# Kernel tuning notes

Hardware: AMD Instinct MI355X
Metric: run time of the kernel (lower is better)

Reference implementation:

```python
import jax, jax.numpy as jnp
import numpy as np

N = 100000
E = 1600000
D_IN = 128
D_OUT = 128

def setup_inputs() -> dict:
    key = jax.random.key(0)
    k1, k2, k3, k4, k5, k6 = jax.random.split(key, 6)
    h = jax.random.normal(k1, (N, D_IN), dtype=jnp.float32)
    # norm ~ deg^{-1/2}; use positive uniform values as stand-in
    norm = jax.random.uniform(k2, (N, 1), dtype=jnp.float32, minval=0.05, maxval=1.0)
    src = jax.random.randint(k3, (E,), 0, N, dtype=jnp.int32)
    dst = jax.random.randint(k4, (E,), 0, N, dtype=jnp.int32)
    weight = jax.random.normal(k5, (D_IN, D_OUT), dtype=jnp.float32) * (2.0 / (D_IN + D_OUT)) ** 0.5
    bias = jnp.zeros((D_OUT,), dtype=jnp.float32)
    return {"h": h, "norm": norm, "src": src, "dst": dst, "weight": weight, "bias": bias}

def reference(h, norm, src, dst, weight, bias):
    n_nodes = h.shape[0]
    hw = h @ weight                      # [N, D_out] dense GEMM
    hw = hw * norm                       # pre-aggregation degree scale
    msgs = hw[src]                       # gather: [E, D_out]
    agg = jax.ops.segment_sum(msgs, dst, num_segments=n_nodes)  # scatter-sum
    out = agg * norm + bias              # post-scale + bias
    return out
```

## Files before the change

### kernel.cpp

```cpp
#include <hip/hip_runtime.h>
#include <hip/hip_bf16.h>
#include <hip/hip_cooperative_groups.h>

namespace cg = cooperative_groups;

#define D 128
#define D4 32
#define CHUNK 6400
#define MAXB 2048
#define NSEG 8
#define SL 4096

typedef __attribute__((ext_vector_type(8))) short bf16x8;
typedef __attribute__((ext_vector_type(8))) unsigned short ushort8;
typedef __attribute__((ext_vector_type(4))) float f32x4;

static __device__ __forceinline__ unsigned short f2bf(float f) {
    unsigned u = __float_as_uint(f);
    u += 0x7FFFu + ((u >> 16) & 1u);
    return (unsigned short)(u >> 16);
}
static __device__ __forceinline__ float bf2f(unsigned short u) {
    return __uint_as_float(((unsigned)u) << 16);
}

__global__ __launch_bounds__(256) void wcvt_kernel(
    const float* __restrict__ W, unsigned short* __restrict__ Wt)
{
    const int idx = blockIdx.x * 256 + threadIdx.x;
    const float4 w = ((const float4*)W)[idx];
    const int k = idx >> 5;
    const int c = (idx & 31) * 4;
    Wt[(c + 0) * 128 + k] = f2bf(w.x);
    Wt[(c + 1) * 128 + k] = f2bf(w.y);
    Wt[(c + 2) * 128 + k] = f2bf(w.z);
    Wt[(c + 3) * 128 + k] = f2bf(w.w);
}

__global__ __launch_bounds__(512) void gemm_mfma_kernel(
    const float* __restrict__ h, const unsigned short* __restrict__ Wt,
    const float* __restrict__ norm, unsigned short* __restrict__ hwb,
    int n_nodes)
{
    __shared__ unsigned short Bs[128 * 136];

    const int t = threadIdx.x;
    const int row0 = blockIdx.x * 128;

    #pragma unroll
    for (int i = 0; i < 4; ++i) {
        const int idx = t + 512 * i;
        const int c = idx >> 4;
        const int k8 = idx & 15;
        *(ushort8*)&Bs[c * 136 + k8 * 8] = ((const ushort8*)Wt)[idx];
    }
    __syncthreads();

    const int wv = t >> 6;
    const int lane = t & 63;
    const int m = lane & 15;
    const int quad = lane >> 4;

    long gra = row0 + wv * 16 + m;
    if (gra >= n_nodes) gra = n_nodes - 1;
    const float* hrow = h + gra * D;

    f32x4 acc[8];
    #pragma unroll
    for (int nt = 0; nt < 8; ++nt) { f32x4 z = {0.f, 0.f, 0.f, 0.f}; acc[nt] = z; }

    #pragma unroll
    for (int kt = 0; kt < 4; ++kt) {
        const float4 a0 = *(const float4*)(hrow + kt * 32 + quad * 8);
        const float4 a1 = *(const float4*)(hrow + kt * 32 + quad * 8 + 4);
        bf16x8 af;
        unsigned short* ap = (unsigned short*)&af;
        ap[0] = f2bf(a0.x); ap[1] = f2bf(a0.y); ap[2] = f2bf(a0.z); ap[3] = f2bf(a0.w);
        ap[4] = f2bf(a1.x); ap[5] = f2bf(a1.y); ap[6] = f2bf(a1.z); ap[7] = f2bf(a1.w);
        #pragma unroll
        for (int nt = 0; nt < 8; ++nt) {
            const bf16x8 bfr = *(const bf16x8*)&Bs[(nt * 16 + m) * 136 + kt * 32 + quad * 8];
            acc[nt] = __builtin_amdgcn_mfma_f32_16x16x32_bf16(af, bfr, acc[nt], 0, 0, 0);
        }
    }

    float nv[4];
    #pragma unroll
    for (int i = 0; i < 4; ++i) {
        const int gr = row0 + wv * 16 + quad * 4 + i;
        nv[i] = (gr < n_nodes) ? norm[gr] : 0.f;
    }

    __syncthreads();
    #pragma unroll
    for (int nt = 0; nt < 8; ++nt) {
        #pragma unroll
        for (int i = 0; i < 4; ++i) {
            const int r = wv * 16 + quad * 4 + i;
            Bs[r * 136 + nt * 16 + m] = f2bf(acc[nt][i] * nv[i]);
        }
    }
    __syncthreads();

    #pragma unroll
    for (int i2 = 0; i2 < 4; ++i2) {
        const int idx = t + 512 * i2;
        const int r = idx >> 4;
        const int c8 = idx & 15;
        const int gr = row0 + r;
        if (gr < n_nodes)
            *(ushort8*)&hwb[(size_t)gr * D + c8 * 8] =
                *(const ushort8*)&Bs[r * 136 + c8 * 8];
    }
}

__global__ __launch_bounds__(1024) void coop_edge_kernel(
    const int* __restrict__ src, const int* __restrict__ dst,
    int* __restrict__ H, int* __restrict__ PS, int* __restrict__ SB,
    int* __restrict__ boff, int* __restrict__ CO,
    unsigned int* __restrict__ ebuf, int* __restrict__ srcs_g,
    const unsigned short* __restrict__ hwb,
    const float* __restrict__ norm, const float* __restrict__ bias,
    float* __restrict__ out,
    int n_edges, int n_nodes, int EB, int NBUCK)
{
    __shared__ int smem[SL + 192];

    cg::grid_group grid = cg::this_grid();
    const int t = threadIdx.x;
    const int g = blockIdx.x;
    const int gid = g * 1024 + t;
    const int glen = (EB + NSEG - 1) / NSEG;
    const int e0 = g * CHUNK;
    const int e1 = min(e0 + CHUNK, n_edges);

    {
        int* lbh = smem;
        for (int i = t; i < MAXB; i += 1024) lbh[i] = 0;
        if (g == 0 && t < 32) {
            ushort4 z; z.x = z.y = z.z = z.w = 0;
            ((ushort4*)(hwb + (size_t)n_nodes * D))[t] = z;
        }
        __syncthreads();
        for (int e = e0 + t; e < e1; e += 1024)
            atomicAdd(&lbh[dst[e] >> 6], 1);
        __syncthreads();
        for (int i = t; i < MAXB; i += 1024) H[(size_t)g * MAXB + i] = lbh[i];
    }
    grid.sync();

    if (gid < NSEG * MAXB) {
        const int seg = gid >> 11;
        const int c = gid & (MAXB - 1);
        const int g0 = seg * glen, g1 = min(g0 + glen, EB);
        int s = 0;
        for (int gg = g0; gg < g1; ++gg) s += H[(size_t)gg * MAXB + c];
        PS[seg * MAXB + c] = s;
    }
    grid.sync();

    if (g == 0) {
        int* tmp = smem;
        const int cA = 2 * t, cB = 2 * t + 1;
        int va = 0, vb = 0;
        #pragma unroll
        for (int sg = 0; sg < NSEG; ++sg) { va += PS[sg * MAXB + cA]; vb += PS[sg * MAXB + cB]; }
        tmp[t] = va + vb;
        __syncthreads();
        for (int ofs = 1; ofs < 1024; ofs <<= 1) {
            const int x = (t >= ofs) ? tmp[t - ofs] : 0;
            __syncthreads();
            tmp[t] += x;
            __syncthreads();
        }
        const int run = tmp[t] - (va + vb);
        boff[cA] = run;
        boff[cB] = run + va;
        if (t == 1023) boff[MAXB] = tmp[1023];
        int sb = run;
        #pragma unroll
        for (int sg = 0; sg < NSEG; ++sg) { SB[sg * MAXB + cA] = sb; sb += PS[sg * MAXB + cA]; }
        sb = run + va;
        #pragma unroll
        for (int sg = 0; sg < NSEG; ++sg) { SB[sg * MAXB + cB] = sb; sb += PS[sg * MAXB + cB]; }
    }
    grid.sync();

    if (gid < NSEG * MAXB) {
        const int seg = gid >> 11;
        const int c = gid & (MAXB - 1);
        const int g0 = seg * glen, g1 = min(g0 + glen, EB);
        int run = SB[seg * MAXB + c];
        for (int gg = g0; gg < g1; ++gg) {
            CO[(size_t)gg * MAXB + c] = run;
            run += H[(size_t)gg * MAXB + c];
        }
    }
    grid.sync();

    {
        int* lbh = smem;
        int* lofs = smem + MAXB;
        for (int i = t; i < MAXB; i += 1024) {
            lbh[i] = 0;
            lofs[i] = CO[(size_t)g * MAXB + i];
        }
        __syncthreads();
        for (int e = e0 + t; e < e1; e += 1024) {
            const int d = dst[e];
            const int bk = d >> 6;
            const int r = atomicAdd(&lbh[bk], 1);
            ebuf[lofs[bk] + r] = (unsigned)src[e] | ((unsigned)(d & 63) << 17);
        }
    }
    grid.sync();

    {
        int* slds = smem;
        int* lcnt = smem + SL;
        int* lcur = smem + SL + 64;
        int* loff = smem + SL + 128;
        const ushort4* hw4 = (const ushort4*)hwb;
        const int grp = t >> 5;
        const int l = t & 31;
        const float4 bs = ((const float4*)bias)[l];

        for (int bkt = g; bkt < NBUCK; bkt += gridDim.x) {
            __syncthreads();
            if (t < 64) lcnt[t] = 0;
            __syncthreads();
            const int w0 = boff[bkt], w1 = boff[bkt + 1];
            const int wlen = w1 - w0;
            const bool uselds = (wlen + 480) <= SL;
            const int gbase = w0 + 448 * bkt;
            const int gn0 = bkt * 64;

            for (int e = w0 + t; e < w1; e += 1024)
                atomicAdd(&lcnt[(ebuf[e] >> 17) & 63], 1);
            __syncthreads();
            if (t < 64) {
                const int c = lcnt[t];
                const int p = (c + 7) & ~7;
                int x = p;
                #pragma unroll
                for (int ofs = 1; ofs < 64; ofs <<= 1) {
                    const int y = __shfl_up(x, ofs, 64);
                    if (t >= ofs) x += y;
                }
                const int base = x - p;
                lcur[t] = base;
                loff[t] = base;
            }
            __syncthreads();
            for (int e = w0 + t; e < w1; e += 1024) {
                const unsigned rec = ebuf[e];
                const int loc = (rec >> 17) & 63;
                const int pos = atomicAdd(&lcur[loc], 1);
                const int sv = (int)(rec & 0x1FFFFu);
                if (uselds) slds[pos] = sv; else srcs_g[gbase + pos] = sv;
            }
            for (int w = t; w < 512; w += 1024) {
                const int ln = w >> 3, k = w & 7;
                const int gn = gn0 + ln;
                if (gn < n_nodes) {
                    const int c = lcnt[ln];
                    const int pad = (8 - (c & 7)) & 7;
                    if (k < pad) {
                        const int pos = loff[ln] + c + k;
                        if (uselds) slds[pos] = n_nodes; else srcs_g[gbase + pos] = n_nodes;
                    }
                }
            }
            __syncthreads();

            #pragma unroll
            for (int nn = 0; nn < 2; ++nn) {
                const int loc = grp * 2 + nn;
                const int gn = gn0 + loc;
                if (gn >= n_nodes) continue;
                const int start = loff[loc];
                const int deg = lcnt[loc];
                const int nb8 = (deg + 7) >> 3;
                float4 acc; acc.x = acc.y = acc.z = acc.w = 0.f;
                int myidx = 0;
                for (int bb = 0; bb < nb8; ++bb) {
                    const int q = bb & 3;
                    if (q == 0) {
                        const int ri = start + bb * 8 + l;
                        myidx = uselds ? slds[ri] : srcs_g[gbase + ri];
                    }
                    ushort4 v[8];
                    #pragma unroll
                    for (int jj = 0; jj < 8; ++jj) {
                        const int s = __shfl(myidx, q * 8 + jj, 32);
                        v[jj] = hw4[(long)s * D4 + l];
                    }
                    #pragma unroll
                    for (int jj = 0; jj < 8; ++jj) {
                        acc.x += bf2f(v[jj].x);
                        acc.y += bf2f(v[jj].y);
                        acc.z += bf2f(v[jj].z);
                        acc.w += bf2f(v[jj].w);
                    }
                }
                const float nv = norm[gn];
                float4 o;
                o.x = acc.x * nv + bs.x;
                o.y = acc.y * nv + bs.y;
                o.z = acc.z * nv + bs.z;
                o.w = acc.w * nv + bs.w;
                ((float4*)out)[(long)gn * D4 + l] = o;
            }
        }
    }
}

__global__ __launch_bounds__(1024) void hist_kernel(
    const int* __restrict__ dst, int* __restrict__ H,
    unsigned short* __restrict__ hwb, int n_edges, int n_nodes)
{
    __shared__ int lbh[MAXB];
    const int t = threadIdx.x;
    const int g = blockIdx.x;
    for (int i = t; i < MAXB; i += 1024) lbh[i] = 0;
    if (g == 0 && t < 32) {
        ushort4 z; z.x = z.y = z.z = z.w = 0;
        ((ushort4*)(hwb + (size_t)n_nodes * D))[t] = z;
    }
    __syncthreads();
    const int e0 = g * CHUNK;
    const int e1 = min(e0 + CHUNK, n_edges);
    for (int e = e0 + t; e < e1; e += 1024) {
        atomicAdd(&lbh[dst[e] >> 6], 1);
    }
    __syncthreads();
    for (int i = t; i < MAXB; i += 1024) {
        H[(size_t)g * MAXB + i] = lbh[i];
    }
}

__global__ __launch_bounds__(256) void chunkscan_local_kernel(
    const int* __restrict__ H, int* __restrict__ CO, int* __restrict__ PS,
    int eb)
{
    const int b = blockIdx.x * 256 + threadIdx.x;
    const int seg = blockIdx.y;
    const int glen = (eb + NSEG - 1) / NSEG;
    const int g0 = seg * glen;
    const int g1 = min(g0 + glen, eb);
    int run = 0;
    for (int g = g0; g < g1; ++g) {
        CO[(size_t)g * MAXB + b] = run;
        run += H[(size_t)g * MAXB + b];
    }
    PS[seg * MAXB + b] = run;
}

__global__ __launch_bounds__(256) void bucket_scan_kernel(
    const int* __restrict__ PS, int* __restrict__ boff, int* __restrict__ SB)
{
    __shared__ int tmp[256];
    const int t = threadIdx.x;
    int v[8];
    int s = 0;
    #pragma unroll
    for (int k = 0; k < 8; ++k) {
        const int i = t * 8 + k;
        int c = 0;
        #pragma unroll
        for (int sg = 0; sg < NSEG; ++sg) c += PS[sg * MAXB + i];
        v[k] = c; s += c;
    }
    tmp[t] = s;
    __syncthreads();
    for (int ofs = 1; ofs < 256; ofs <<= 1) {
        int x = (t >= ofs) ? tmp[t - ofs] : 0;
        __syncthreads();
        tmp[t] += x;
        __syncthreads();
    }
    int run = tmp[t] - s;
    #pragma unroll
    for (int k = 0; k < 8; ++k) {
        const int i = t * 8 + k;
        boff[i] = run;
        int sb = run;
        #pragma unroll
        for (int sg = 0; sg < NSEG; ++sg) {
            SB[sg * MAXB + i] = sb;
            sb += PS[sg * MAXB + i];
        }
        run += v[k];
    }
    if (t == 255) boff[MAXB] = run;
}

__global__ __launch_bounds__(1024) void bscatter_kernel(
    const int* __restrict__ src, const int* __restrict__ dst,
    const int* __restrict__ CO, const int* __restrict__ SB,
    unsigned int* __restrict__ ebuf, int n_edges, int eb)
{
    __shared__ int lbh[MAXB];
    __shared__ int lofs[MAXB];
    const int t = threadIdx.x;
    const int g = blockIdx.x;
    const int glen = (eb + NSEG - 1) / NSEG;
    const int seg = g / glen;
    for (int i = t; i < MAXB; i += 1024) {
        lbh[i] = 0;
        lofs[i] = SB[seg * MAXB + i] + CO[(size_t)g * MAXB + i];
    }
    __syncthreads();
    const int e0 = g * CHUNK;
    const int e1 = min(e0 + CHUNK, n_edges);
    for (int e = e0 + t; e < e1; e += 1024) {
        const int d = dst[e];
        const int bk = d >> 6;
        const int r = atomicAdd(&lbh[bk], 1);
        ebuf[lofs[bk] + r] = (unsigned)src[e] | ((unsigned)(d & 63) << 17);
    }
}

__global__ __launch_bounds__(256) void fillagg_kernel(
    const unsigned int* __restrict__ ebuf, const int* __restrict__ boff,
    int* __restrict__ srcs_g, const unsigned short* __restrict__ hwb,
    const float* __restrict__ norm, const float* __restrict__ bias,
    float* __restrict__ out, int n_nodes)
{
    __shared__ int slds[SL];
    __shared__ int lcnt[64];
    __shared__ int lcur[64];
    __shared__ int loff[64];
    const int t = threadIdx.x;
    const int b = blockIdx.x;
    const int gn0 = b * 64;

    if (t < 64) lcnt[t] = 0;
    __syncthreads();
    const int w0 = boff[b], w1 = boff[b + 1];
    const int wlen = w1 - w0;
    const bool uselds = (wlen + 480) <= SL;
    const int gbase = w0 + 448 * b;

    for (int e = w0 + t; e < w1; e += 256) {
        atomicAdd(&lcnt[(ebuf[e] >> 17) & 63], 1);
    }
    __syncthreads();
    if (t < 64) {
        const int c = lcnt[t];
        const int p = (c + 7) & ~7;
        int x = p;
        #pragma unroll
        for (int ofs = 1; ofs < 64; ofs <<= 1) {
            const int y = __shfl_up(x, ofs, 64);
            if (t >= ofs) x += y;
        }
        const int base = x - p;
        lcur[t] = base;
        loff[t] = base;
    }
    __syncthreads();
    for (int e = w0 + t; e < w1; e += 256) {
        const unsigned rec = ebuf[e];
        const int loc = (rec >> 17) & 63;
        const int pos = atomicAdd(&lcur[loc], 1);
        const int sv = (int)(rec & 0x1FFFFu);
        if (uselds) slds[pos] = sv; else srcs_g[gbase + pos] = sv;
    }
    for (int w = t; w < 512; w += 256) {
        const int ln = w >> 3, k = w & 7;
        const int gn = gn0 + ln;
        if (gn < n_nodes) {
            const int c = lcnt[ln];
            const int pad = (8 - (c & 7)) & 7;
            if (k < pad) {
                const int pos = loff[ln] + c + k;
                if (uselds) slds[pos] = n_nodes; else srcs_g[gbase + pos] = n_nodes;
            }
        }
    }
    __syncthreads();

    const ushort4* hw4 = (const ushort4*)hwb;
    const int grp = t >> 5;
    const int l = t & 31;
    const float4 bs = ((const float4*)bias)[l];
    for (int nn = 0; nn < 8; ++nn) {
        const int loc = grp * 8 + nn;
        const int gn = gn0 + loc;
        if (gn >= n_nodes) continue;
        const int start = loff[loc];
        const int deg = lcnt[loc];
        const int nb8 = (deg + 7) >> 3;
        float4 acc; acc.x = acc.y = acc.z = acc.w = 0.f;
        int myidx = 0;
        for (int bb = 0; bb < nb8; ++bb) {
            const int q = bb & 3;
            if (q == 0) {
                const int ri = start + bb * 8 + l;
                myidx = uselds ? slds[ri] : srcs_g[gbase + ri];
            }
            ushort4 v[8];
            #pragma unroll
            for (int jj = 0; jj < 8; ++jj) {
                const int s = __shfl(myidx, q * 8 + jj, 32);
                v[jj] = hw4[(long)s * D4 + l];
            }
            #pragma unroll
            for (int jj = 0; jj < 8; ++jj) {
                acc.x += bf2f(v[jj].x);
                acc.y += bf2f(v[jj].y);
                acc.z += bf2f(v[jj].z);
                acc.w += bf2f(v[jj].w);
            }
        }
        const float nv = norm[gn];
        float4 o;
        o.x = acc.x * nv + bs.x;
        o.y = acc.y * nv + bs.y;
        o.z = acc.z * nv + bs.z;
        o.w = acc.w * nv + bs.w;
        ((float4*)out)[(long)gn * D4 + l] = o;
    }
}

__global__ __launch_bounds__(256) void scatter_kernel(
    const unsigned short* __restrict__ hwb, const int* __restrict__ src,
    const int* __restrict__ dst, float* __restrict__ out, int n_edges)
{
    const int idx = blockIdx.x * 256 + threadIdx.x;
    if (idx >= n_edges * D4) return;
    const int e = idx >> 5;
    const int g = idx & 31;
    const int s = src[e];
    const int d = dst[e];
    const ushort4 v = ((const ushort4*)hwb)[(long)s * D4 + g];
    float* o = out + (long)d * D + g * 4;
    atomicAdd(o + 0, bf2f(v.x));
    atomicAdd(o + 1, bf2f(v.y));
    atomicAdd(o + 2, bf2f(v.z));
    atomicAdd(o + 3, bf2f(v.w));
}

__global__ __launch_bounds__(256) void finalize_kernel(
    float* __restrict__ out, const float* __restrict__ norm,
    const float* __restrict__ bias, int n_nodes)
{
    const int idx = blockIdx.x * 256 + threadIdx.x;
    if (idx >= n_nodes * D4) return;
    const int n = idx >> 5;
    const int g = idx & 31;
    float4 v = ((float4*)out)[idx];
    const float nv = norm[n];
    const float4 b = ((const float4*)bias)[g];
    v.x = v.x * nv + b.x;
    v.y = v.y * nv + b.y;
    v.z = v.z * nv + b.z;
    v.w = v.w * nv + b.w;
    ((float4*)out)[idx] = v;
}

extern "C" void kernel_launch(void* const* d_in, const int* in_sizes, int n_in,
                              void* d_out, int out_size, void* d_ws, size_t ws_size,
                              hipStream_t stream) {
    const float* h    = (const float*)d_in[0];
    const float* norm = (const float*)d_in[1];
    const int*   src  = (const int*)d_in[2];
    const int*   dst  = (const int*)d_in[3];
    const float* W    = (const float*)d_in[4];
    const float* bias = (const float*)d_in[5];
    float* out = (float*)d_out;

    const int n_nodes = in_sizes[1];
    const int n_edges = in_sizes[2];

    const int NBUCK = (n_nodes + 63) >> 6;
    const int EB    = (n_edges + CHUNK - 1) / CHUNK;
    const int srcs_len = n_edges + 448 * NBUCK + 64;

    size_t p = 0;
    auto take = [&](size_t bytes) {
        size_t cur = p;
        p += (bytes + 255) & ~(size_t)255;
        return cur;
    };
    const size_t hwb_off  = take(((size_t)n_nodes + 1) * D * sizeof(unsigned short));
    const size_t wt_off   = take((size_t)D * D * sizeof(unsigned short));
    const size_t srcs_off = take((size_t)srcs_len * sizeof(int));
    const size_t ebuf_off = take((size_t)n_edges * sizeof(unsigned int));
    const size_t boff_off = take((MAXB + 1) * sizeof(int));
    const size_t H_off    = take((size_t)EB * MAXB * sizeof(int));
    const size_t PS_off   = take((size_t)NSEG * MAXB * sizeof(int));
    const size_t SB_off   = take((size_t)NSEG * MAXB * sizeof(int));
    const size_t CO_off   = take((size_t)EB * MAXB * sizeof(int));
    const size_t needed = p;

    char* ws = (char*)d_ws;
    unsigned short* hwb = (unsigned short*)(ws + hwb_off);
    unsigned short* Wt  = (unsigned short*)(ws + wt_off);

    wcvt_kernel<<<16, 256, 0, stream>>>(W, Wt);
    gemm_mfma_kernel<<<(n_nodes + 127) / 128, 512, 0, stream>>>(h, Wt, norm, hwb, n_nodes);

    static int s_max_coop_blocks = -1;
    if (s_max_coop_blocks < 0) {
        int nb = 0;
        if (hipOccupancyMaxActiveBlocksPerMultiprocessor(&nb, coop_edge_kernel, 1024, 0)
            != hipSuccess) nb = 0;
        int dev = 0;
        hipGetDevice(&dev);
        int ncu = 0;
        if (hipDeviceGetAttribute(&ncu, hipDeviceAttributeMultiprocessorCount, dev)
            != hipSuccess) ncu = 0;
        s_max_coop_blocks = nb * ncu;
    }

    const bool ws_ok = (ws_size >= needed) && (NBUCK <= MAXB) && (n_nodes <= 131072);
    const bool coop_ok = ws_ok && EB >= 16 && EB <= 512 && EB <= s_max_coop_blocks;

    if (coop_ok) {
        int* srcs  = (int*)(ws + srcs_off);
        unsigned int* ebuf = (unsigned int*)(ws + ebuf_off);
        int* boff  = (int*)(ws + boff_off);
        int* H     = (int*)(ws + H_off);
        int* PS    = (int*)(ws + PS_off);
        int* SBp   = (int*)(ws + SB_off);
        int* CO    = (int*)(ws + CO_off);

        int ne = n_edges, nn = n_nodes, eb = EB, nbk = NBUCK;
        void* args[] = {
            (void*)&src, (void*)&dst, (void*)&H, (void*)&PS, (void*)&SBp,
            (void*)&boff, (void*)&CO, (void*)&ebuf, (void*)&srcs, (void*)&hwb,
            (void*)&norm, (void*)&bias, (void*)&out,
            (void*)&ne, (void*)&nn, (void*)&eb, (void*)&nbk
        };
        hipLaunchCooperativeKernel((void*)coop_edge_kernel, dim3(EB), dim3(1024),
                                   args, 0, stream);
    } else if (ws_ok && EB <= 1024) {
        int* srcs  = (int*)(ws + srcs_off);
        unsigned int* ebuf = (unsigned int*)(ws + ebuf_off);
        int* boff  = (int*)(ws + boff_off);
        int* H     = (int*)(ws + H_off);
        int* PS    = (int*)(ws + PS_off);
        int* SBp   = (int*)(ws + SB_off);
        int* CO    = (int*)(ws + CO_off);

        hist_kernel<<<EB, 1024, 0, stream>>>(dst, H, hwb, n_edges, n_nodes);
        chunkscan_local_kernel<<<dim3(MAXB / 256, NSEG), 256, 0, stream>>>(H, CO, PS, EB);
        bucket_scan_kernel<<<1, 256, 0, stream>>>(PS, boff, SBp);
        bscatter_kernel<<<EB, 1024, 0, stream>>>(src, dst, CO, SBp, ebuf, n_edges, EB);
        fillagg_kernel<<<NBUCK, 256, 0, stream>>>(ebuf, boff, srcs, hwb, norm, bias,
                                                  out, n_nodes);
    } else {
        hipMemsetAsync(d_out, 0, (size_t)out_size * sizeof(float), stream);
        const int work = n_edges * D4;
        scatter_kernel<<<(work + 255) / 256, 256, 0, stream>>>(hwb, src, dst, out, n_edges);
        const int work2 = n_nodes * D4;
        finalize_kernel<<<(work2 + 255) / 256, 256, 0, stream>>>(out, norm, bias, n_nodes);
    }
}
```

Measured before the change: 227.4 us.

## Keep edge records in registers across grid syncs and drop CO pass

Edges are now loaded once into registers during the histogram phase, and the LDS atomic rank is kept so the scatter phase needs neither a second read of src/dst nor a second atomic pass. The separate chunk-offset pass, its CO buffer and one grid.sync are removed: each block rebuilds its own offsets by summing H over earlier blocks in its segment. In the bucket phase, records read from ebuf are also held in registers between the count and place steps. Float-to-bf16 conversion now uses a packed two-value intrinsic. In exchange, register pressure rises and per-block offset work grows with segment length. All of this assumes CHUNK fits in KSLOT*1024 edges and each bucket in 4096 records.

```diff
diff --git a/kernel.cpp b/kernel.cpp
--- a/kernel.cpp
+++ b/kernel.cpp
@@ -7,6 +7,7 @@
 #define D 128
 #define D4 32
 #define CHUNK 6400
+#define KSLOT 7
 #define MAXB 2048
 #define NSEG 8
 #define SL 4096
@@ -15,13 +16,13 @@
 typedef __attribute__((ext_vector_type(8))) unsigned short ushort8;
 typedef __attribute__((ext_vector_type(4))) float f32x4;
 
-static __device__ __forceinline__ unsigned short f2bf(float f) {
-    unsigned u = __float_as_uint(f);
-    u += 0x7FFFu + ((u >> 16) & 1u);
-    return (unsigned short)(u >> 16);
-}
 static __device__ __forceinline__ float bf2f(unsigned short u) {
     return __uint_as_float(((unsigned)u) << 16);
+}
+static __device__ __forceinline__ unsigned pk2(float x, float y) {
+    float2 f; f.x = x; f.y = y;
+    __hip_bfloat162 b = __float22bfloat162_rn(f);
+    return *(unsigned*)&b;
 }
 
 __global__ __launch_bounds__(256) void wcvt_kernel(
@@ -31,10 +32,12 @@
     const float4 w = ((const float4*)W)[idx];
     const int k = idx >> 5;
     const int c = (idx & 31) * 4;
-    Wt[(c + 0) * 128 + k] = f2bf(w.x);
-    Wt[(c + 1) * 128 + k] = f2bf(w.y);
-    Wt[(c + 2) * 128 + k] = f2bf(w.z);
-    Wt[(c + 3) * 128 + k] = f2bf(w.w);
+    const unsigned q01 = pk2(w.x, w.y);
+    const unsigned q23 = pk2(w.z, w.w);
+    Wt[(c + 0) * 128 + k] = (unsigned short)(q01 & 0xFFFFu);
+    Wt[(c + 1) * 128 + k] = (unsigned short)(q01 >> 16);
+    Wt[(c + 2) * 128 + k] = (unsigned short)(q23 & 0xFFFFu);
+    Wt[(c + 3) * 128 + k] = (unsigned short)(q23 >> 16);
 }
 
 __global__ __launch_bounds__(512) void gemm_mfma_kernel(
@@ -74,9 +77,11 @@
         const float4 a0 = *(const float4*)(hrow + kt * 32 + quad * 8);
         const float4 a1 = *(const float4*)(hrow + kt * 32 + quad * 8 + 4);
         bf16x8 af;
-        unsigned short* ap = (unsigned short*)&af;
-        ap[0] = f2bf(a0.x); ap[1] = f2bf(a0.y); ap[2] = f2bf(a0.z); ap[3] = f2bf(a0.w);
-        ap[4] = f2bf(a1.x); ap[5] = f2bf(a1.y); ap[6] = f2bf(a1.z); ap[7] = f2bf(a1.w);
+        unsigned* aw = (unsigned*)&af;
+        aw[0] = pk2(a0.x, a0.y);
+        aw[1] = pk2(a0.z, a0.w);
+        aw[2] = pk2(a1.x, a1.y);
+        aw[3] = pk2(a1.z, a1.w);
         #pragma unroll
         for (int nt = 0; nt < 8; ++nt) {
             const bf16x8 bfr = *(const bf16x8*)&Bs[(nt * 16 + m) * 136 + kt * 32 + quad * 8];
@@ -94,11 +99,13 @@
     __syncthreads();
     #pragma unroll
     for (int nt = 0; nt < 8; ++nt) {
-        #pragma unroll
-        for (int i = 0; i < 4; ++i) {
-            const int r = wv * 16 + quad * 4 + i;
-            Bs[r * 136 + nt * 16 + m] = f2bf(acc[nt][i] * nv[i]);
-        }
+        const unsigned q01 = pk2(acc[nt][0] * nv[0], acc[nt][1] * nv[1]);
+        const unsigned q23 = pk2(acc[nt][2] * nv[2], acc[nt][3] * nv[3]);
+        const int rb = wv * 16 + quad * 4;
+        Bs[(rb + 0) * 136 + nt * 16 + m] = (unsigned short)(q01 & 0xFFFFu);
+        Bs[(rb + 1) * 136 + nt * 16 + m] = (unsigned short)(q01 >> 16);
+        Bs[(rb + 2) * 136 + nt * 16 + m] = (unsigned short)(q23 & 0xFFFFu);
+        Bs[(rb + 3) * 136 + nt * 16 + m] = (unsigned short)(q23 >> 16);
     }
     __syncthreads();
 
@@ -117,7 +124,7 @@
 __global__ __launch_bounds__(1024) void coop_edge_kernel(
     const int* __restrict__ src, const int* __restrict__ dst,
     int* __restrict__ H, int* __restrict__ PS, int* __restrict__ SB,
-    int* __restrict__ boff, int* __restrict__ CO,
+    int* __restrict__ boff,
     unsigned int* __restrict__ ebuf, int* __restrict__ srcs_g,
     const unsigned short* __restrict__ hwb,
     const float* __restrict__ norm, const float* __restrict__ bias,
@@ -134,6 +141,7 @@
     const int e0 = g * CHUNK;
     const int e1 = min(e0 + CHUNK, n_edges);
 
+    int ed[KSLOT], es[KSLOT], er[KSLOT];
     {
         int* lbh = smem;
         for (int i = t; i < MAXB; i += 1024) lbh[i] = 0;
@@ -142,8 +150,15 @@
             ((ushort4*)(hwb + (size_t)n_nodes * D))[t] = z;
         }
         __syncthreads();
-        for (int e = e0 + t; e < e1; e += 1024)
-            atomicAdd(&lbh[dst[e] >> 6], 1);
+        #pragma unroll
+        for (int k = 0; k < KSLOT; ++k) {
+            const int e = e0 + t + 1024 * k;
+            if (e < e1) {
+                ed[k] = dst[e];
+                es[k] = src[e];
+                er[k] = atomicAdd(&lbh[ed[k] >> 6], 1);
+            } else { ed[k] = -1; es[k] = 0; er[k] = 0; }
+        }
         __syncthreads();
         for (int i = t; i < MAXB; i += 1024) H[(size_t)g * MAXB + i] = lbh[i];
     }
@@ -186,31 +201,21 @@
     }
     grid.sync();
 
-    if (gid < NSEG * MAXB) {
-        const int seg = gid >> 11;
-        const int c = gid & (MAXB - 1);
-        const int g0 = seg * glen, g1 = min(g0 + glen, EB);
-        int run = SB[seg * MAXB + c];
-        for (int gg = g0; gg < g1; ++gg) {
-            CO[(size_t)gg * MAXB + c] = run;
-            run += H[(size_t)gg * MAXB + c];
-        }
-    }
-    grid.sync();
-
     {
-        int* lbh = smem;
-        int* lofs = smem + MAXB;
+        int* lofs = smem;
+        const int seg = g / glen;
+        const int g0s = seg * glen;
         for (int i = t; i < MAXB; i += 1024) {
-            lbh[i] = 0;
-            lofs[i] = CO[(size_t)g * MAXB + i];
+            int run = SB[seg * MAXB + i];
+            for (int gg = g0s; gg < g; ++gg) run += H[(size_t)gg * MAXB + i];
+            lofs[i] = run;
         }
         __syncthreads();
-        for (int e = e0 + t; e < e1; e += 1024) {
-            const int d = dst[e];
-            const int bk = d >> 6;
-            const int r = atomicAdd(&lbh[bk], 1);
-            ebuf[lofs[bk] + r] = (unsigned)src[e] | ((unsigned)(d & 63) << 17);
+        #pragma unroll
+        for (int k = 0; k < KSLOT; ++k) {
+            if (ed[k] >= 0)
+                ebuf[lofs[ed[k] >> 6] + er[k]] =
+                    (unsigned)es[k] | ((unsigned)(ed[k] & 63) << 17);
         }
     }
     grid.sync();
@@ -235,8 +240,20 @@
             const int gbase = w0 + 448 * bkt;
             const int gn0 = bkt * 64;
 
-            for (int e = w0 + t; e < w1; e += 1024)
-                atomicAdd(&lcnt[(ebuf[e] >> 17) & 63], 1);
+            unsigned rc[4];
+            if (uselds) {
+                #pragma unroll
+                for (int k = 0; k < 4; ++k) {
+                    const int e = w0 + t + k * 1024;
+                    if (e < w1) {
+                        rc[k] = ebuf[e];
+                        atomicAdd(&lcnt[(rc[k] >> 17) & 63], 1);
+                    }
+                }
+            } else {
+                for (int e = w0 + t; e < w1; e += 1024)
+                    atomicAdd(&lcnt[(ebuf[e] >> 17) & 63], 1);
+            }
             __syncthreads();
             if (t < 64) {
                 const int c = lcnt[t];
@@ -252,12 +269,24 @@
                 loff[t] = base;
             }
             __syncthreads();
-            for (int e = w0 + t; e < w1; e += 1024) {
-                const unsigned rec = ebuf[e];
-                const int loc = (rec >> 17) & 63;
-                const int pos = atomicAdd(&lcur[loc], 1);
-                const int sv = (int)(rec & 0x1FFFFu);
-                if (uselds) slds[pos] = sv; else srcs_g[gbase + pos] = sv;
+            if (uselds) {
+                #pragma unroll
+                for (int k = 0; k < 4; ++k) {
+                    const int e = w0 + t + k * 1024;
+                    if (e < w1) {
+                        const unsigned rec = rc[k];
+                        const int loc = (rec >> 17) & 63;
+                        const int pos = atomicAdd(&lcur[loc], 1);
+                        slds[pos] = (int)(rec & 0x1FFFFu);
+                    }
+                }
+            } else {
+                for (int e = w0 + t; e < w1; e += 1024) {
+                    const unsigned rec = ebuf[e];
+                    const int loc = (rec >> 17) & 63;
+                    const int pos = atomicAdd(&lcur[loc], 1);
+                    srcs_g[gbase + pos] = (int)(rec & 0x1FFFFu);
+                }
             }
             for (int w = t; w < 512; w += 1024) {
                 const int ln = w >> 3, k = w & 7;
@@ -625,12 +654,11 @@
         int* H     = (int*)(ws + H_off);
         int* PS    = (int*)(ws + PS_off);
         int* SBp   = (int*)(ws + SB_off);
-        int* CO    = (int*)(ws + CO_off);
 
         int ne = n_edges, nn = n_nodes, eb = EB, nbk = NBUCK;
         void* args[] = {
             (void*)&src, (void*)&dst, (void*)&H, (void*)&PS, (void*)&SBp,
-            (void*)&boff, (void*)&CO, (void*)&ebuf, (void*)&srcs, (void*)&hwb,
+            (void*)&boff, (void*)&ebuf, (void*)&srcs, (void*)&hwb,
             (void*)&norm, (void*)&bias, (void*)&out,
             (void*)&ne, (void*)&nn, (void*)&eb, (void*)&nbk
         };
```

After: 229.3 us. About the same (+0.8%).
